# Optimization experiments

Hardware: AMD Instinct MI355X
Metric: run time of the kernel (lower is better)

## Reference

```python
import jax, jax.numpy as jnp
import numpy as np

B, N, NPOINT, NSAMPLE = 8, 16384, 512, 64
RADIUS = 0.1
C_IN = 64
DIMS = [64, 64, 128]


def setup_inputs() -> dict:
    key = jax.random.key(0)
    ks = jax.random.split(key, 8)
    xyz = jax.random.uniform(ks[0], (B, N, 3), jnp.float32)          # points in unit cube
    features = jax.random.normal(ks[1], (B, C_IN, N), jnp.float32)   # (B, C, N) per GroupGatherByIndex
    dims = [3 + C_IN] + DIMS                                         # use_xyz_feature adds 3
    out = {"xyz": xyz, "features": features}
    for i in range(3):
        out[f"W{i+1}"] = jax.random.normal(ks[2 + i], (dims[i], dims[i + 1]), jnp.float32) / np.sqrt(dims[i])
        out[f"b{i+1}"] = jnp.zeros((dims[i + 1],), jnp.float32)
    return out


def furthest_point_sampling(xyz, npoint):
    # Iterative FPS starting at index 0 (matches CUDA kernel semantics).
    Bq, Nq, _ = xyz.shape
    barange = jnp.arange(Bq)

    def step(carry, _):
        dists, last = carry
        p = xyz[barange, last]                       # (B, 3)
        d = jnp.sum((xyz - p[:, None, :]) ** 2, -1)  # (B, N)
        dists = jnp.minimum(dists, d)
        nxt = jnp.argmax(dists, axis=1).astype(jnp.int32)
        return (dists, nxt), nxt

    init = (jnp.full((Bq, Nq), 1e10, xyz.dtype), jnp.zeros((Bq,), jnp.int32))
    _, idxs = jax.lax.scan(step, init, None, length=npoint - 1)
    return jnp.concatenate([jnp.zeros((Bq, 1), jnp.int32), idxs.T], axis=1)  # (B, npoint)


def ball_query(new_xyz, xyz, radius, nsample):
    # For each centroid, first nsample in-ball indices (ascending), padded with first hit.
    Nq = xyz.shape[1]
    d2 = jnp.sum((new_xyz[:, :, None, :] - xyz[:, None, :, :]) ** 2, -1)  # (B, npoint, N)
    cand = jnp.where(d2 < radius * radius, jnp.arange(Nq, dtype=jnp.int32), Nq)
    cand = jnp.sort(cand, axis=-1)[..., :nsample]                          # (B, npoint, nsample)
    first = jnp.where(cand[..., :1] == Nq, 0, cand[..., :1])
    return jnp.where(cand == Nq, first, cand)


def reference(xyz, features, W1, b1, W2, b2, W3, b3):
    fps_idx = furthest_point_sampling(xyz, NPOINT)                  # (B, npoint)
    new_xyz = jax.vmap(lambda p, i: p[i])(xyz, fps_idx)             # (B, npoint, 3)
    idx = ball_query(new_xyz, xyz, RADIUS, NSAMPLE)                 # (B, npoint, nsample)
    grouped_xyz = jax.vmap(lambda p, i: p[i])(xyz, idx)             # (B, npoint, nsample, 3)
    centered = grouped_xyz - new_xyz[:, :, None, :]                 # centroid subtract
    feats_n = jnp.transpose(features, (0, 2, 1))                    # (B, N, C)
    grouped_f = jax.vmap(lambda f, i: f[i])(feats_n, idx)           # (B, npoint, nsample, C)
    h = jnp.concatenate([centered, grouped_f], axis=-1)             # (B, npoint, nsample, 3+C)
    for W, b in ((W1, b1), (W2, b2), (W3, b3)):                     # pointwise 1x1-conv MLP + ReLU
        h = jax.nn.relu(h @ W + b)
    return jnp.max(h, axis=2)                                       # max-pool over nsample -> (B, npoint, C_out)
```

## Files before the change

kernel.cpp:

```cpp
#include <hip/hip_runtime.h>

#define NB 8
#define NPTS 16384
#define NPOINT 512
#define NSAMPLE 64
#define CIN 64

__global__ __launch_bounds__(512) void fps_transpose_kernel(
    const float* __restrict__ xyz, const float* __restrict__ feats,
    int* __restrict__ fps_idx, float* __restrict__ feats_t)
{
    __shared__ float t[64][65];
    __shared__ __align__(16) float s_rd[8];
    __shared__ __align__(16) int   s_ri[2][8];
    __shared__ float s_px[2][8], s_py[2][8], s_pz[2][8];

    if (blockIdx.x >= NB) {
        int blk = blockIdx.x - NB;
        int b = blk & 7;
        int tile = blk >> 3;
        int n0 = tile * 64;
        int cc = threadIdx.x & 63, rr = threadIdx.x >> 6;
        const float* fb = feats + (size_t)b * CIN * NPTS;
        #pragma unroll
        for (int k = 0; k < 8; ++k) {
            int c = rr + k * 8;
            t[c][cc] = fb[(size_t)c * NPTS + n0 + cc];
        }
        __syncthreads();
        float* fo = feats_t + ((size_t)b * NPTS + n0) * CIN;
        #pragma unroll
        for (int k = 0; k < 8; ++k) {
            int n = rr + k * 8;
            fo[n * CIN + cc] = t[cc][n];
        }
        return;
    }

    const int b = blockIdx.x;
    const int tid = threadIdx.x;
    const int wv = tid >> 6, ln = tid & 63;
    const float* xb = xyz + (size_t)b * NPTS * 3;

    float px[32], py[32], pz[32], dd[32];
    #pragma unroll
    for (int k = 0; k < 32; ++k) {
        int i = tid + k * 512;
        px[k] = xb[3 * i + 0];
        py[k] = xb[3 * i + 1];
        pz[k] = xb[3 * i + 2];
        dd[k] = 1e10f;
    }
    if (tid == 0) fps_idx[b * NPOINT] = 0;
    if (ln == 0) { s_ri[0][wv] = 0x7fffffff; s_ri[1][wv] = 0x7fffffff; }
    float cx = xb[0], cy = xb[1], cz = xb[2];
    __syncthreads();

    for (int j = 1; j < NPOINT; ++j) {
        const int p = j & 1;
        float bm = -1.0f;
        #pragma unroll
        for (int k = 0; k < 32; ++k) {
            float dx = __fsub_rn(px[k], cx);
            float dy = __fsub_rn(py[k], cy);
            float dz = __fsub_rn(pz[k], cz);
            float d = __fadd_rn(__fadd_rn(__fmul_rn(dx, dx), __fmul_rn(dy, dy)), __fmul_rn(dz, dz));
            float nd = fminf(dd[k], d);
            dd[k] = nd;
            bm = fmaxf(bm, nd);
        }
        #pragma unroll
        for (int off = 1; off < 64; off <<= 1)
            bm = fmaxf(bm, __shfl_xor(bm, off));
        if (ln == 0) s_rd[wv] = bm;
        __syncthreads();
        float4 r0 = *(const float4*)&s_rd[0];
        float4 r1 = *(const float4*)&s_rd[4];
        float bmax = fmaxf(fmaxf(fmaxf(r0.x, r0.y), fmaxf(r0.z, r0.w)),
                           fmaxf(fmaxf(r1.x, r1.y), fmaxf(r1.z, r1.w)));
        int mi = 0x7fffffff;
        float cpx = 0.f, cpy = 0.f, cpz = 0.f;
        if (bm == bmax) {
            #pragma unroll
            for (int k = 0; k < 32; ++k) {
                if (dd[k] == bmax) {
                    int cand = tid + k * 512;
                    if (cand < mi) { mi = cand; cpx = px[k]; cpy = py[k]; cpz = pz[k]; }
                }
            }
        }
        int wmi = mi;
        #pragma unroll
        for (int off = 1; off < 64; off <<= 1)
            wmi = min(wmi, __shfl_xor(wmi, off));
        if (mi == wmi && wmi != 0x7fffffff) {
            s_ri[p][wv] = mi;
            s_px[p][wv] = cpx; s_py[p][wv] = cpy; s_pz[p][wv] = cpz;
        }
        if (ln == 0) s_ri[1 - p][wv] = 0x7fffffff;
        __syncthreads();
        int4 ra = *(const int4*)&s_ri[p][0];
        int4 rb = *(const int4*)&s_ri[p][4];
        int ch = min(min(min(ra.x, ra.y), min(ra.z, ra.w)),
                     min(min(rb.x, rb.y), min(rb.z, rb.w)));
        int wvw = 7;
        wvw = (rb.z == ch) ? 6 : wvw;
        wvw = (rb.y == ch) ? 5 : wvw;
        wvw = (rb.x == ch) ? 4 : wvw;
        wvw = (ra.w == ch) ? 3 : wvw;
        wvw = (ra.z == ch) ? 2 : wvw;
        wvw = (ra.y == ch) ? 1 : wvw;
        wvw = (ra.x == ch) ? 0 : wvw;
        cx = s_px[p][wvw]; cy = s_py[p][wvw]; cz = s_pz[p][wvw];
        if (tid == 0) fps_idx[b * NPOINT + j] = ch;
    }
}

__global__ __launch_bounds__(64) void ball_kernel(
    const float* __restrict__ xyz, const int* __restrict__ fps_idx, int* __restrict__ ball_idx)
{
    const float R2 = (float)(0.1 * 0.1);
    int blk = blockIdx.x;
    int b = blk & 7, j = blk >> 3;
    int lane = threadIdx.x;
    int cent = b * NPOINT + j;
    const float* xb = xyz + (size_t)b * NPTS * 3;
    int cidx = fps_idx[cent];
    float cx = xb[3 * cidx + 0];
    float cy = xb[3 * cidx + 1];
    float cz = xb[3 * cidx + 2];

    __shared__ int slots[64];
    int cnt = 0;
    for (int base = 0; base < NPTS; base += 64) {
        int i = base + lane;
        float dx = __fsub_rn(xb[3 * i + 0], cx);
        float dy = __fsub_rn(xb[3 * i + 1], cy);
        float dz = __fsub_rn(xb[3 * i + 2], cz);
        float d2 = __fadd_rn(__fadd_rn(__fmul_rn(dx, dx), __fmul_rn(dy, dy)), __fmul_rn(dz, dz));
        bool inb = d2 < R2;
        unsigned long long m = __ballot(inb);
        int pre = (int)__popcll(m & ((1ull << lane) - 1ull));
        int slot = cnt + pre;
        if (inb && slot < NSAMPLE) slots[slot] = i;
        cnt += (int)__popcll(m);
        if (cnt >= NSAMPLE) break;
    }
    __syncthreads();
    int first = (cnt > 0) ? slots[0] : 0;
    int v = (lane < cnt) ? slots[lane] : first;
    ball_idx[(size_t)cent * NSAMPLE + lane] = v;
}

__global__ __launch_bounds__(64) void mlp_kernel(
    const float* __restrict__ xyz, const float* __restrict__ feats_t,
    const int* __restrict__ fps_idx, const int* __restrict__ ball_idx,
    const float* __restrict__ W1, const float* __restrict__ b1,
    const float* __restrict__ W2, const float* __restrict__ b2,
    const float* __restrict__ W3, const float* __restrict__ b3,
    float* __restrict__ out)
{
    int blk = blockIdx.x;
    int b = blk & 7, j = blk >> 3;
    int s = threadIdx.x;
    int cent = b * NPOINT + j;

    __shared__ float X[64][68];

    int i = ball_idx[(size_t)cent * NSAMPLE + s];
    int cidx = fps_idx[cent];
    const float* cp = xyz + ((size_t)b * NPTS + cidx) * 3;
    float cx = cp[0], cy = cp[1], cz = cp[2];
    const float* pp = xyz + ((size_t)b * NPTS + i) * 3;
    X[s][64] = pp[0] - cx;
    X[s][65] = pp[1] - cy;
    X[s][66] = pp[2] - cz;
    const float4* fr = (const float4*)(feats_t + ((size_t)b * NPTS + i) * CIN);
    #pragma unroll
    for (int q = 0; q < 16; ++q) *(float4*)&X[s][q * 4] = fr[q];

    float acc[64];
    #pragma unroll
    for (int o = 0; o < 64; ++o) acc[o] = b1[o];
    for (int c = 0; c < 67; ++c) {
        float xc = X[s][c];
        const float* w = W1 + ((c < 64) ? (c + 3) : (c - 64)) * 64;
        #pragma unroll
        for (int o = 0; o < 64; ++o) acc[o] = fmaf(xc, w[o], acc[o]);
    }
    #pragma unroll
    for (int o = 0; o < 64; ++o) X[s][o] = fmaxf(acc[o], 0.0f);

    #pragma unroll
    for (int o = 0; o < 64; ++o) acc[o] = b2[o];
    for (int c = 0; c < 64; ++c) {
        float xc = X[s][c];
        const float* w = W2 + c * 64;
        #pragma unroll
        for (int o = 0; o < 64; ++o) acc[o] = fmaf(xc, w[o], acc[o]);
    }
    #pragma unroll
    for (int o = 0; o < 64; ++o) X[s][o] = fmaxf(acc[o], 0.0f);

    float h3[128];
    #pragma unroll
    for (int o = 0; o < 128; ++o) h3[o] = b3[o];
    for (int c = 0; c < 64; ++c) {
        float xc = X[s][c];
        const float* w = W3 + c * 128;
        #pragma unroll
        for (int o = 0; o < 128; ++o) h3[o] = fmaf(xc, w[o], h3[o]);
    }

    #pragma unroll
    for (int o = 0; o < 128; ++o) {
        float v = fmaxf(h3[o], 0.0f);
        #pragma unroll
        for (int off = 1; off < 64; off <<= 1) v = fmaxf(v, __shfl_xor(v, off));
        h3[o] = v;
    }
    if (s == 0) {
        float* op = out + (size_t)cent * 128;
        #pragma unroll
        for (int o = 0; o < 128; o += 4) {
            float4 v = make_float4(h3[o], h3[o + 1], h3[o + 2], h3[o + 3]);
            *(float4*)&op[o] = v;
        }
    }
}

extern "C" void kernel_launch(void* const* d_in, const int* in_sizes, int n_in,
                              void* d_out, int out_size, void* d_ws, size_t ws_size,
                              hipStream_t stream) {
    const float* xyz   = (const float*)d_in[0];
    const float* feats = (const float*)d_in[1];
    const float* W1 = (const float*)d_in[2];
    const float* b1 = (const float*)d_in[3];
    const float* W2 = (const float*)d_in[4];
    const float* b2 = (const float*)d_in[5];
    const float* W3 = (const float*)d_in[6];
    const float* b3 = (const float*)d_in[7];
    float* out = (float*)d_out;

    char* ws = (char*)d_ws;
    int*   fps_idx  = (int*)ws;
    int*   ball_idx = (int*)(ws + 16384);
    float* feats_t  = (float*)(ws + 16384 + 1048576);

    fps_transpose_kernel<<<NB + NB * (NPTS / 64), 512, 0, stream>>>(xyz, feats, fps_idx, feats_t);
    ball_kernel<<<NB * NPOINT, 64, 0, stream>>>(xyz, fps_idx, ball_idx);
    mlp_kernel<<<NB * NPOINT, 64, 0, stream>>>(xyz, feats_t, fps_idx, ball_idx,
                                               W1, b1, W2, b2, W3, b3, out);
}
```

Baseline: 1.404 ms.

## Restructure FPS loop: packed-f32 math, DPP reductions, single barrier per step

Rewrites the furthest-point-sampling iteration. Each thread now owns a contiguous block of 32 points, loaded as float4 and packed into v2f so the distance math uses v_pk_add/v_pk_mul. Wave reductions use DPP row ops plus readlane instead of shuffles. Each wave publishes one (max, index) pair, which removes one of the two __syncthreads per step. The new centroid coordinates are then reloaded from global memory by index instead of being passed through shared memory. In exchange, each step now adds a dependent global load on the critical path, and packed math drops the explicit round-to-nearest intrinsics.

```diff
diff --git a/kernel.cpp b/kernel.cpp
--- a/kernel.cpp
+++ b/kernel.cpp
@@ -6,14 +6,58 @@
 #define NSAMPLE 64
 #define CIN 64
 
-__global__ __launch_bounds__(512) void fps_transpose_kernel(
+typedef float v2f __attribute__((ext_vector_type(2)));
+
+__device__ __forceinline__ v2f pk_add(v2f a, v2f b) {
+    v2f d;
+    asm("v_pk_add_f32 %0, %1, %2" : "=v"(d) : "v"(a), "v"(b));
+    return d;
+}
+__device__ __forceinline__ v2f pk_mul(v2f a, v2f b) {
+    v2f d;
+    asm("v_pk_mul_f32 %0, %1, %2" : "=v"(d) : "v"(a), "v"(b));
+    return d;
+}
+
+template <int CTRL>
+__device__ __forceinline__ float dpp_f(float x) {
+    int xi = __builtin_bit_cast(int, x);
+    int yi = __builtin_amdgcn_update_dpp(xi, xi, CTRL, 0xF, 0xF, false);
+    return __builtin_bit_cast(float, yi);
+}
+template <int CTRL>
+__device__ __forceinline__ int dpp_i(int x) {
+    return __builtin_amdgcn_update_dpp(x, x, CTRL, 0xF, 0xF, false);
+}
+
+__device__ __forceinline__ float wave_max_f(float x) {
+    x = fmaxf(x, dpp_f<0x111>(x));
+    x = fmaxf(x, dpp_f<0x112>(x));
+    x = fmaxf(x, dpp_f<0x114>(x));
+    x = fmaxf(x, dpp_f<0x118>(x));
+    x = fmaxf(x, dpp_f<0x142>(x));
+    x = fmaxf(x, dpp_f<0x143>(x));
+    return x;
+}
+__device__ __forceinline__ int wave_min_i(int x) {
+    x = min(x, dpp_i<0x111>(x));
+    x = min(x, dpp_i<0x112>(x));
+    x = min(x, dpp_i<0x114>(x));
+    x = min(x, dpp_i<0x118>(x));
+    x = min(x, dpp_i<0x142>(x));
+    x = min(x, dpp_i<0x143>(x));
+    return x;
+}
+
+#define CMB(va, ia, vb, ib) { bool t_ = ((vb) > (va)) || (((vb) == (va)) && ((ib) < (ia))); \
+                              if (t_) { (va) = (vb); (ia) = (ib); } }
+
+__global__ __launch_bounds__(512, 1) void fps_transpose_kernel(
     const float* __restrict__ xyz, const float* __restrict__ feats,
     int* __restrict__ fps_idx, float* __restrict__ feats_t)
 {
     __shared__ float t[64][65];
-    __shared__ __align__(16) float s_rd[8];
-    __shared__ __align__(16) int   s_ri[2][8];
-    __shared__ float s_px[2][8], s_py[2][8], s_pz[2][8];
+    __shared__ __align__(16) int s_pair[2][8][2];
 
     if (blockIdx.x >= NB) {
         int blk = blockIdx.x - NB;
@@ -41,77 +85,86 @@
     const int tid = threadIdx.x;
     const int wv = tid >> 6, ln = tid & 63;
     const float* xb = xyz + (size_t)b * NPTS * 3;
-
-    float px[32], py[32], pz[32], dd[32];
-    #pragma unroll
-    for (int k = 0; k < 32; ++k) {
-        int i = tid + k * 512;
-        px[k] = xb[3 * i + 0];
-        py[k] = xb[3 * i + 1];
-        pz[k] = xb[3 * i + 2];
-        dd[k] = 1e10f;
+    const int base = tid * 32;
+
+    v2f px2[16], py2[16], pz2[16];
+    float dd[32];
+    {
+        const float4* xb4 = (const float4*)(xb + (size_t)base * 3);
+        #pragma unroll
+        for (int q = 0; q < 8; ++q) {
+            float4 f0 = xb4[3 * q + 0];
+            float4 f1 = xb4[3 * q + 1];
+            float4 f2 = xb4[3 * q + 2];
+            px2[2 * q + 0] = (v2f){f0.x, f0.w};
+            py2[2 * q + 0] = (v2f){f0.y, f1.x};
+            pz2[2 * q + 0] = (v2f){f0.z, f1.y};
+            px2[2 * q + 1] = (v2f){f1.z, f2.y};
+            py2[2 * q + 1] = (v2f){f1.w, f2.z};
+            pz2[2 * q + 1] = (v2f){f2.x, f2.w};
+        }
+        #pragma unroll
+        for (int k = 0; k < 32; ++k) dd[k] = 1e10f;
     }
     if (tid == 0) fps_idx[b * NPOINT] = 0;
-    if (ln == 0) { s_ri[0][wv] = 0x7fffffff; s_ri[1][wv] = 0x7fffffff; }
     float cx = xb[0], cy = xb[1], cz = xb[2];
     __syncthreads();
 
     for (int j = 1; j < NPOINT; ++j) {
         const int p = j & 1;
+        v2f ncx = (v2f){-cx, -cx};
+        v2f ncy = (v2f){-cy, -cy};
+        v2f ncz = (v2f){-cz, -cz};
         float bm = -1.0f;
         #pragma unroll
-        for (int k = 0; k < 32; ++k) {
-            float dx = __fsub_rn(px[k], cx);
-            float dy = __fsub_rn(py[k], cy);
-            float dz = __fsub_rn(pz[k], cz);
-            float d = __fadd_rn(__fadd_rn(__fmul_rn(dx, dx), __fmul_rn(dy, dy)), __fmul_rn(dz, dz));
-            float nd = fminf(dd[k], d);
-            dd[k] = nd;
-            bm = fmaxf(bm, nd);
-        }
-        #pragma unroll
-        for (int off = 1; off < 64; off <<= 1)
-            bm = fmaxf(bm, __shfl_xor(bm, off));
-        if (ln == 0) s_rd[wv] = bm;
+        for (int k = 0; k < 16; ++k) {
+            v2f dx = pk_add(px2[k], ncx);
+            v2f dy = pk_add(py2[k], ncy);
+            v2f dz = pk_add(pz2[k], ncz);
+            v2f sx = pk_mul(dx, dx);
+            v2f sy = pk_mul(dy, dy);
+            v2f sz = pk_mul(dz, dz);
+            v2f s1 = pk_add(sx, sy);
+            v2f d2 = pk_add(s1, sz);
+            float n0 = fminf(dd[2 * k + 0], d2.x);
+            float n1 = fminf(dd[2 * k + 1], d2.y);
+            dd[2 * k + 0] = n0;
+            dd[2 * k + 1] = n1;
+            bm = fmaxf(fmaxf(bm, n0), n1);
+        }
+        float wm = wave_max_f(bm);
+        float wmax = __builtin_bit_cast(float,
+            __builtin_amdgcn_readlane(__builtin_bit_cast(int, wm), 63));
+        int mi = 0x7fffffff;
+        #pragma unroll
+        for (int k = 31; k >= 0; --k)
+            mi = (dd[k] == wmax) ? (base + k) : mi;
+        int rm = wave_min_i(mi);
+        int wave_mi = __builtin_amdgcn_readlane(rm, 63);
+        if (ln == 0) {
+            s_pair[p][wv][0] = __builtin_bit_cast(int, wmax);
+            s_pair[p][wv][1] = wave_mi;
+        }
         __syncthreads();
-        float4 r0 = *(const float4*)&s_rd[0];
-        float4 r1 = *(const float4*)&s_rd[4];
-        float bmax = fmaxf(fmaxf(fmaxf(r0.x, r0.y), fmaxf(r0.z, r0.w)),
-                           fmaxf(fmaxf(r1.x, r1.y), fmaxf(r1.z, r1.w)));
-        int mi = 0x7fffffff;
-        float cpx = 0.f, cpy = 0.f, cpz = 0.f;
-        if (bm == bmax) {
-            #pragma unroll
-            for (int k = 0; k < 32; ++k) {
-                if (dd[k] == bmax) {
-                    int cand = tid + k * 512;
-                    if (cand < mi) { mi = cand; cpx = px[k]; cpy = py[k]; cpz = pz[k]; }
-                }
-            }
-        }
-        int wmi = mi;
-        #pragma unroll
-        for (int off = 1; off < 64; off <<= 1)
-            wmi = min(wmi, __shfl_xor(wmi, off));
-        if (mi == wmi && wmi != 0x7fffffff) {
-            s_ri[p][wv] = mi;
-            s_px[p][wv] = cpx; s_py[p][wv] = cpy; s_pz[p][wv] = cpz;
-        }
-        if (ln == 0) s_ri[1 - p][wv] = 0x7fffffff;
-        __syncthreads();
-        int4 ra = *(const int4*)&s_ri[p][0];
-        int4 rb = *(const int4*)&s_ri[p][4];
-        int ch = min(min(min(ra.x, ra.y), min(ra.z, ra.w)),
-                     min(min(rb.x, rb.y), min(rb.z, rb.w)));
-        int wvw = 7;
-        wvw = (rb.z == ch) ? 6 : wvw;
-        wvw = (rb.y == ch) ? 5 : wvw;
-        wvw = (rb.x == ch) ? 4 : wvw;
-        wvw = (ra.w == ch) ? 3 : wvw;
-        wvw = (ra.z == ch) ? 2 : wvw;
-        wvw = (ra.y == ch) ? 1 : wvw;
-        wvw = (ra.x == ch) ? 0 : wvw;
-        cx = s_px[p][wvw]; cy = s_py[p][wvw]; cz = s_pz[p][wvw];
+        int4 q0 = *(const int4*)&s_pair[p][0][0];
+        int4 q1 = *(const int4*)&s_pair[p][2][0];
+        int4 q2 = *(const int4*)&s_pair[p][4][0];
+        int4 q3 = *(const int4*)&s_pair[p][6][0];
+        float v0 = __builtin_bit_cast(float, q0.x); int i0 = q0.y;
+        float v1 = __builtin_bit_cast(float, q0.z); int i1 = q0.w;
+        float v2 = __builtin_bit_cast(float, q1.x); int i2 = q1.y;
+        float v3 = __builtin_bit_cast(float, q1.z); int i3 = q1.w;
+        float v4 = __builtin_bit_cast(float, q2.x); int i4 = q2.y;
+        float v5 = __builtin_bit_cast(float, q2.z); int i5 = q2.w;
+        float v6 = __builtin_bit_cast(float, q3.x); int i6 = q3.y;
+        float v7 = __builtin_bit_cast(float, q3.z); int i7 = q3.w;
+        CMB(v0, i0, v1, i1); CMB(v2, i2, v3, i3);
+        CMB(v4, i4, v5, i5); CMB(v6, i6, v7, i7);
+        CMB(v0, i0, v2, i2); CMB(v4, i4, v6, i6);
+        CMB(v0, i0, v4, i4);
+        int ch = __builtin_amdgcn_readfirstlane(i0);
+        const float* cp = xb + 3 * ch;
+        cx = cp[0]; cy = cp[1]; cz = cp[2];
         if (tid == 0) fps_idx[b * NPOINT + j] = ch;
     }
 }
```

Result: faster. 1.244 ms (-11.4%).
